# Kernel optimization log

Measured on AMD Instinct MI355X. Metric: run time of the kernel, lower is better.

## Reference

```python
import jax, jax.numpy as jnp
import numpy as np

TEMPERATURE = 0.5
EPS = 1e-8  # matches torch CosineSimilarity eps


def setup_inputs() -> dict:
    key = jax.random.key(0)
    k1, k2 = jax.random.split(key)
    N, D = 4096, 256
    z1 = jax.random.normal(k1, (N, D), dtype=jnp.float32)
    z2 = jax.random.normal(k2, (N, D), dtype=jnp.float32)
    return {"z1": z1, "z2": z2}


def reference(z1, z2):
    N = z1.shape[0]
    z = jnp.concatenate([z1, z2], axis=0)            # [2N, D]
    norm = jnp.linalg.norm(z, axis=-1, keepdims=True)
    zn = z / jnp.maximum(norm, EPS)                  # L2-normalized
    sim = (zn @ zn.T) / TEMPERATURE                  # [2N, 2N] cosine sim / temp
    # mask self-similarity on the diagonal
    diag = jnp.eye(2 * N, dtype=bool)
    sim = jnp.where(diag, -jnp.inf, sim)
    # positive pair labels: row i pairs with i+N (first half) or i-N (second half)
    labels = jnp.concatenate([jnp.arange(N) + N, jnp.arange(N)])
    logp = jax.nn.log_softmax(sim, axis=-1)
    loss = -jnp.mean(logp[jnp.arange(2 * N), labels])
    return loss
```

## Files before the change

### kernel.cpp

```cpp
#include <hip/hip_runtime.h>
#include <hip/hip_bf16.h>


#define NROWS 8192
#define NHALF 4096
#define DDIM  256

typedef __bf16 bf16;
typedef __bf16 bf16x4 __attribute__((ext_vector_type(4)));
typedef __bf16 bf16x8 __attribute__((ext_vector_type(8)));
typedef float  f32x4  __attribute__((ext_vector_type(4)));

__constant__ const float kTwoLog2e = 2.8853900817779268f;
__constant__ const float kLn2      = 0.6931471805599453f;

__device__ __forceinline__ const float* zrow(const float* z1, const float* z2, int r) {
  return (r < NHALF) ? (z1 + (size_t)r * DDIM) : (z2 + (size_t)(r - NHALF) * DDIM);
}

__global__ void k_normalize(const float* __restrict__ z1, const float* __restrict__ z2,
                            bf16* __restrict__ zn, float* __restrict__ invn,
                            float* __restrict__ rowsum) {
  const int wave = threadIdx.x >> 6, lane = threadIdx.x & 63;
  const int row = blockIdx.x * 4 + wave;
  const float* src = zrow(z1, z2, row);
  f32x4 v = *(const f32x4*)(src + lane * 4);
  float ss = v.x * v.x + v.y * v.y + v.z * v.z + v.w * v.w;
#pragma unroll
  for (int off = 1; off < 64; off <<= 1) ss += __shfl_xor(ss, off);
  const float inv = 1.0f / fmaxf(sqrtf(ss), 1e-8f);
  bf16x4 o;
  o.x = (bf16)(v.x * inv); o.y = (bf16)(v.y * inv);
  o.z = (bf16)(v.z * inv); o.w = (bf16)(v.w * inv);
  *(bf16x4*)(zn + (size_t)row * DDIM + lane * 4) = o;
  if (lane == 0) { invn[row] = inv; rowsum[row] = 0.0f; }
}

#define BMG 128
#define NTILES 2080

typedef const __attribute__((address_space(1))) unsigned int* as1_u32p;
typedef __attribute__((address_space(3))) unsigned int* as3_u32p;

__device__ __forceinline__ void load_lds16(const void* g, void* l) {
  __builtin_amdgcn_global_load_lds((as1_u32p)g, (as3_u32p)l, 16, 0, 0);
}

__global__ __launch_bounds__(256, 2) void k_gram(const bf16* __restrict__ zn,
                                                 float* __restrict__ rowsum) {
  __shared__ __align__(16) unsigned char ldsb[2][64 * 512];
  const int tid  = threadIdx.x;
  const int wave = tid >> 6, lane = tid & 63;
  const int quad = lane >> 4, l15 = lane & 15;

  const int kb = blockIdx.x;
  int I = (int)((129.0f - sqrtf((float)(16641 - 8 * kb))) * 0.5f);
  while ((I + 1) * (129 - (I + 1)) / 2 <= kb) ++I;
  while (I * (129 - I) / 2 > kb) --I;
  const int J = I + (kb - I * (129 - I) / 2);
  const bool diag = (I == J);
  const int R0 = I * BMG + wave * 32;
  const int C0 = J * BMG;

  {
    const unsigned char* s0 = (const unsigned char*)(zn + (size_t)C0 * DDIM);
#pragma unroll
    for (int j = 0; j < 8; ++j) {
      const int p = (wave * 8 + j) * 64 + lane;
      const int r = p >> 5;
      const int q = (p & 31) ^ (r & 15);
      load_lds16(s0 + r * 512 + q * 16, &ldsb[0][(wave * 8 + j) * 1024]);
    }
  }

  bf16x8 a[2][8];
#pragma unroll
  for (int s = 0; s < 2; ++s) {
    const bf16x8* ap = (const bf16x8*)(zn + (size_t)(R0 + s * 16 + l15) * DDIM);
#pragma unroll
    for (int kk = 0; kk < 8; ++kk) a[s][kk] = ap[kk * 4 + quad];
  }

  {
    const unsigned char* s1 = (const unsigned char*)(zn + (size_t)(C0 + 64) * DDIM);
#pragma unroll
    for (int j = 0; j < 8; ++j) {
      const int p = (wave * 8 + j) * 64 + lane;
      const int r = p >> 5;
      const int q = (p & 31) ^ (r & 15);
      load_lds16(s1 + r * 512 + q * 16, &ldsb[1][(wave * 8 + j) * 1024]);
    }
  }
  __builtin_amdgcn_sched_barrier(0);

  float sum[2][4] = {{0.f, 0.f, 0.f, 0.f}, {0.f, 0.f, 0.f, 0.f}};
  float csum[2][4];
  const f32x4 zero4 = {0.f, 0.f, 0.f, 0.f};

#pragma unroll
  for (int h = 0; h < 2; ++h) {
    if (h == 0) {
      asm volatile("s_waitcnt vmcnt(8)" ::: "memory");
    } else {
      asm volatile("s_waitcnt vmcnt(0)" ::: "memory");
    }
    __builtin_amdgcn_s_barrier();
    __builtin_amdgcn_sched_barrier(0);

    const unsigned char* bp = ldsb[h];

    f32x4 acc[2][4];
#pragma unroll
    for (int s = 0; s < 2; ++s)
#pragma unroll
      for (int cs = 0; cs < 4; ++cs) acc[s][cs] = zero4;

    __builtin_amdgcn_s_setprio(1);
#pragma unroll
    for (int kk = 0; kk < 8; ++kk) {
      bf16x8 b[4];
#pragma unroll
      for (int cs = 0; cs < 4; ++cs) {
        const int rb = cs * 16 + l15;
        const int sl = (kk * 4 + quad) ^ (rb & 15);
        b[cs] = *(const bf16x8*)(bp + rb * 512 + sl * 16);
      }
#pragma unroll
      for (int s = 0; s < 2; ++s)
#pragma unroll
        for (int cs = 0; cs < 4; ++cs)
          acc[s][cs] =
              __builtin_amdgcn_mfma_f32_16x16x32_bf16(a[s][kk], b[cs], acc[s][cs], 0, 0, 0);
    }
    __builtin_amdgcn_s_setprio(0);

#pragma unroll
    for (int cs = 0; cs < 4; ++cs) {
      float c = 0.f;
#pragma unroll
      for (int s = 0; s < 2; ++s)
#pragma unroll
        for (int r = 0; r < 4; ++r) {
          const float e = __builtin_amdgcn_exp2f(acc[s][cs][r] * kTwoLog2e);
          sum[s][r] += e;
          c += e;
        }
      csum[h][cs] = c;
    }
  }

#pragma unroll
  for (int s = 0; s < 2; ++s)
#pragma unroll
    for (int r = 0; r < 4; ++r) {
      float v = sum[s][r];
      v += __shfl_xor(v, 1); v += __shfl_xor(v, 2);
      v += __shfl_xor(v, 4); v += __shfl_xor(v, 8);
      if (l15 == 0) atomicAdd(&rowsum[R0 + s * 16 + quad * 4 + r], v);
    }

  if (!diag) {
#pragma unroll
    for (int h = 0; h < 2; ++h)
#pragma unroll
      for (int cs = 0; cs < 4; ++cs) {
        float v = csum[h][cs];
        v += __shfl_xor(v, 16); v += __shfl_xor(v, 32);
        if (quad == 0) atomicAdd(&rowsum[C0 + h * 64 + cs * 16 + l15], v);
      }
  }
}

__global__ void k_finalize(const float* __restrict__ z1, const float* __restrict__ z2,
                           const bf16* __restrict__ zn, const float* __restrict__ invn,
                           const float* __restrict__ rowsum, float* __restrict__ contrib) {
  const int wave = threadIdx.x >> 6, lane = threadIdx.x & 63;
  const int row = blockIdx.x * 4 + wave;
  const int pr = (row < NHALF) ? row + NHALF : row - NHALF;

  f32x4 a4 = *(const f32x4*)(zrow(z1, z2, row) + lane * 4);
  f32x4 b4 = *(const f32x4*)(zrow(z1, z2, pr) + lane * 4);
  bf16x4 nb = *(const bf16x4*)(zn + (size_t)row * DDIM + lane * 4);

  float pd = a4.x * b4.x + a4.y * b4.y + a4.z * b4.z + a4.w * b4.w;
  float f0 = (float)nb.x, f1 = (float)nb.y, f2 = (float)nb.z, f3 = (float)nb.w;
  float nd = f0 * f0 + f1 * f1 + f2 * f2 + f3 * f3;
#pragma unroll
  for (int off = 1; off < 64; off <<= 1) {
    pd += __shfl_xor(pd, off);
    nd += __shfl_xor(nd, off);
  }
  if (lane == 0) {
    const float p = 2.0f * pd * invn[row] * invn[pr];
    const float dexp = __builtin_amdgcn_exp2f(kTwoLog2e * nd);
    const float lse = __builtin_amdgcn_logf(rowsum[row] - dexp) * kLn2;
    contrib[row] = lse - p;
  }
}

__global__ void k_reduce(const float* __restrict__ contrib, float* __restrict__ out) {
  const int wave = threadIdx.x >> 6, lane = threadIdx.x & 63;
  float acc = 0.0f;
  for (int i = threadIdx.x; i < NROWS; i += 256) acc += contrib[i];
#pragma unroll
  for (int off = 1; off < 64; off <<= 1) acc += __shfl_xor(acc, off);
  __shared__ float wsum[4];
  if (lane == 0) wsum[wave] = acc;
  __syncthreads();
  if (threadIdx.x == 0)
    out[0] = (wsum[0] + wsum[1] + wsum[2] + wsum[3]) * (1.0f / (float)NROWS);
}

extern "C" void kernel_launch(void* const* d_in, const int* in_sizes, int n_in,
                              void* d_out, int out_size, void* d_ws, size_t ws_size,
                              hipStream_t stream) {
  const float* z1 = (const float*)d_in[0];
  const float* z2 = (const float*)d_in[1];
  unsigned char* ws = (unsigned char*)d_ws;

  bf16* zn = (bf16*)ws;
  float* invn = (float*)(ws + (size_t)NROWS * DDIM * sizeof(bf16));
  float* rowsum = invn + NROWS;
  float* contrib = rowsum + NROWS;

  hipLaunchKernelGGL(k_normalize, dim3(NROWS / 4), dim3(256), 0, stream, z1, z2, zn, invn, rowsum);
  hipLaunchKernelGGL(k_gram, dim3(NTILES), dim3(256), 0, stream, zn, rowsum);
  hipLaunchKernelGGL(k_finalize, dim3(NROWS / 4), dim3(256), 0, stream, z1, z2, zn, invn, rowsum,
                     contrib);
  hipLaunchKernelGGL(k_reduce, dim3(1), dim3(256), 0, stream, contrib, (float*)d_out);
}
```

Measured before the change: 118.9 us.

## Make gram blocks persistent over a cyclic tile band with double-buffered LDS pipeline

The symmetric gram kernel moves from 2080 one-tile blocks to 512 blocks. Each block keeps its A row-block in registers and walks a cyclic band of column tiles, streaming B tiles through double-buffered LDS with asynchronous loads. This amortises A loads and launch overhead and overlaps DMA with MFMA, but adds per-tile barriers and column atomics. Separately, the final reduction kernel is removed: finalize now reduces per block and atomically adds into the output, which normalize zeroes.

```diff
diff --git a/kernel.cpp b/kernel.cpp
--- a/kernel.cpp
+++ b/kernel.cpp
@@ -20,7 +20,7 @@
 
 __global__ void k_normalize(const float* __restrict__ z1, const float* __restrict__ z2,
                             bf16* __restrict__ zn, float* __restrict__ invn,
-                            float* __restrict__ rowsum) {
+                            float* __restrict__ rowsum, float* __restrict__ out) {
   const int wave = threadIdx.x >> 6, lane = threadIdx.x & 63;
   const int row = blockIdx.x * 4 + wave;
   const float* src = zrow(z1, z2, row);
@@ -34,16 +34,17 @@
   o.z = (bf16)(v.z * inv); o.w = (bf16)(v.w * inv);
   *(bf16x4*)(zn + (size_t)row * DDIM + lane * 4) = o;
   if (lane == 0) { invn[row] = inv; rowsum[row] = 0.0f; }
-}
-
-#define BMG 128
-#define NTILES 2080
+  if (blockIdx.x == 0 && threadIdx.x == 0) out[0] = 0.0f;
+}
+
+#define NBLK 512
 
 typedef const __attribute__((address_space(1))) unsigned int* as1_u32p;
 typedef __attribute__((address_space(3))) unsigned int* as3_u32p;
 
 __device__ __forceinline__ void load_lds16(const void* g, void* l) {
-  __builtin_amdgcn_global_load_lds((as1_u32p)g, (as3_u32p)l, 16, 0, 0);
+  __builtin_amdgcn_global_lo\
+ad_lds((as1_u32p)g, (as3_u32p)l, 16, 0, 0);
 }
 
 __global__ __launch_bounds__(256, 2) void k_gram(const bf16* __restrict__ zn,
@@ -53,25 +54,30 @@
   const int wave = tid >> 6, lane = tid & 63;
   const int quad = lane >> 4, l15 = lane & 15;
 
-  const int kb = blockIdx.x;
-  int I = (int)((129.0f - sqrtf((float)(16641 - 8 * kb))) * 0.5f);
-  while ((I + 1) * (129 - (I + 1)) / 2 <= kb) ++I;
-  while (I * (129 - I) / 2 > kb) --I;
-  const int J = I + (kb - I * (129 - I) / 2);
-  const bool diag = (I == J);
-  const int R0 = I * BMG + wave * 32;
-  const int C0 = J * BMG;
-
-  {
-    const unsigned char* s0 = (const unsigned char*)(zn + (size_t)C0 * DDIM);
+  const int I      = blockIdx.x >> 3;
+  const int chunk  = blockIdx.x & 7;
+  const int base_d = chunk * 4;
+  const int n      = (chunk == 7 && I < 32) ? 10 : 8;
+  const int R0     = I * 128 + wave * 32;
+
+  auto cbase = [&](int t) -> int {
+    const int d = base_d + (t >> 1);
+    const int J = (I + d) & 63;
+    return J * 128 + (t & 1) * 64;
+  };
+  auto issue_dma = [&](int t, int b) {
+    const unsigned char* s = (const unsigned char*)(zn + (size_t)cbase(t) * DDIM);
 #pragma unroll
     for (int j = 0; j < 8; ++j) {
       const int p = (wave * 8 + j) * 64 + lane;
       const int r = p >> 5;
       const int q = (p & 31) ^ (r & 15);
-      load_lds16(s0 + r * 512 + q * 16, &ldsb[0][(wave * 8 + j) * 1024]);
-    }
-  }
+      load_lds16(s + r * 512 + q * 16, &ldsb[b][(wave * 8 + j) * 1024]);
+    }
+  };
+
+  issue_dma(0, 0);
+  __builtin_amdgcn_sched_barrier(0);
 
   bf16x8 a[2][8];
 #pragma unroll
@@ -80,34 +86,21 @@
 #pragma unroll
     for (int kk = 0; kk < 8; ++kk) a[s][kk] = ap[kk * 4 + quad];
   }
-
-  {
-    const unsigned char* s1 = (const unsigned char*)(zn + (size_t)(C0 + 64) * DDIM);
-#pragma unroll
-    for (int j = 0; j < 8; ++j) {
-      const int p = (wave * 8 + j) * 64 + lane;
-      const int r = p >> 5;
-      const int q = (p & 31) ^ (r & 15);
-      load_lds16(s1 + r * 512 + q * 16, &ldsb[1][(wave * 8 + j) * 1024]);
-    }
-  }
   __builtin_amdgcn_sched_barrier(0);
 
+  issue_dma(1, 1);
+  __builtin_amdgcn_sched_barrier(0);
+
   float sum[2][4] = {{0.f, 0.f, 0.f, 0.f}, {0.f, 0.f, 0.f, 0.f}};
-  float csum[2][4];
   const f32x4 zero4 = {0.f, 0.f, 0.f, 0.f};
 
-#pragma unroll
-  for (int h = 0; h < 2; ++h) {
-    if (h == 0) {
-      asm volatile("s_waitcnt vmcnt(8)" ::: "memory");
-    } else {
-      asm volatile("s_waitcnt vmcnt(0)" ::: "memory");
-    }
+  for (int t = 0; t < n; ++t) {
+    if (t == n - 1) asm volatile("s_waitcnt vmcnt(0)" ::: "memory");
+    else            asm volatile("s_waitcnt vmcnt(8)" ::: "memory");
     __builtin_amdgcn_s_barrier();
     __builtin_amdgcn_sched_barrier(0);
 
-    const unsigned char* bp = ldsb[h];
+    const unsigned char* bp = ldsb[t & 1];
 
     f32x4 acc[2][4];
 #pragma unroll
@@ -134,6 +127,8 @@
     }
     __builtin_amdgcn_s_setprio(0);
 
+    const bool dg = (chunk == 0 && t < 2);
+    const int cb = cbase(t);
 #pragma unroll
     for (int cs = 0; cs < 4; ++cs) {
       float c = 0.f;
@@ -145,7 +140,17 @@
           sum[s][r] += e;
           c += e;
         }
-      csum[h][cs] = c;
+      if (!dg) {
+        c += __shfl_xor(c, 16); c += __shfl_xor(c, 32);
+        if (quad == 0) atomicAdd(&rowsum[cb + cs * 16 + l15], c);
+      }
+    }
+
+    __builtin_amdgcn_s_barrier();
+    __builtin_amdgcn_sched_barrier(0);
+    if (t + 2 < n) {
+      issue_dma(t + 2, t & 1);
+      __builtin_amdgcn_sched_barrier(0);
     }
   }
 
@@ -158,22 +163,11 @@
       v += __shfl_xor(v, 4); v += __shfl_xor(v, 8);
       if (l15 == 0) atomicAdd(&rowsum[R0 + s * 16 + quad * 4 + r], v);
     }
-
-  if (!diag) {
-#pragma unroll
-    for (int h = 0; h < 2; ++h)
-#pragma unroll
-      for (int cs = 0; cs < 4; ++cs) {
-        float v = csum[h][cs];
-        v += __shfl_xor(v, 16); v += __shfl_xor(v, 32);
-        if (quad == 0) atomicAdd(&rowsum[C0 + h * 64 + cs * 16 + l15], v);
-      }
-  }
 }
 
 __global__ void k_finalize(const float* __restrict__ z1, const float* __restrict__ z2,
                            const bf16* __restrict__ zn, const float* __restrict__ invn,
-                           const float* __restrict__ rowsum, float* __restrict__ contrib) {
+                           const float* __restrict__ rowsum, float* __restrict__ out) {
   const int wave = threadIdx.x >> 6, lane = threadIdx.x & 63;
   const int row = blockIdx.x * 4 + wave;
   const int pr = (row < NHALF) ? row + NHALF : row - NHALF;
@@ -190,25 +184,16 @@
     pd += __shfl_xor(pd, off);
     nd += __shfl_xor(nd, off);
   }
+  __shared__ float wsum[4];
   if (lane == 0) {
     const float p = 2.0f * pd * invn[row] * invn[pr];
     const float dexp = __builtin_amdgcn_exp2f(kTwoLog2e * nd);
     const float lse = __builtin_amdgcn_logf(rowsum[row] - dexp) * kLn2;
-    contrib[row] = lse - p;
-  }
-}
-
-__global__ void k_reduce(const float* __restrict__ contrib, float* __restrict__ out) {
-  const int wave = threadIdx.x >> 6, lane = threadIdx.x & 63;
-  float acc = 0.0f;
-  for (int i = threadIdx.x; i < NROWS; i += 256) acc += contrib[i];
-#pragma unroll
-  for (int off = 1; off < 64; off <<= 1) acc += __shfl_xor(acc, off);
-  __shared__ float wsum[4];
-  if (lane == 0) wsum[wave] = acc;
+    wsum[wave] = lse - p;
+  }
   __syncthreads();
   if (threadIdx.x == 0)
-    out[0] = (wsum[0] + wsum[1] + wsum[2] + wsum[3]) * (1.0f / (float)NROWS);
+    atomicAdd(out, (wsum[0] + wsum[1] + wsum[2] + wsum[3]) * (1.0f / (float)NROWS));
 }
 
 extern "C" void kernel_launch(void* const* d_in, const int* in_sizes, int n_in,
@@ -221,11 +206,11 @@
   bf16* zn = (bf16*)ws;
   float* invn = (float*)(ws + (size_t)NROWS * DDIM * sizeof(bf16));
   float* rowsum = invn + NROWS;
-  float* contrib = rowsum + NROWS;
-
-  hipLaunchKernelGGL(k_normalize, dim3(NROWS / 4), dim3(256), 0, stream, z1, z2, zn, invn, rowsum);
-  hipLaunchKernelGGL(k_gram, dim3(NTILES), dim3(256), 0, stream, zn, rowsum);
+  float* out = (float*)d_out;
+
+  hipLaunchKernelGGL(k_normalize, dim3(NROWS / 4), dim3(256), 0, stream, z1, z2, zn, invn, rowsum,
+                     out);
+  hipLaunchKernelGGL(k_gram, dim3(NBLK), dim3(256), 0, stream, zn, rowsum);
   hipLaunchKernelGGL(k_finalize, dim3(NROWS / 4), dim3(256), 0, stream, z1, z2, zn, invn, rowsum,
-                     contrib);
-  hipLaunchKernelGGL(k_reduce, dim3(1), dim3(256), 0, stream, contrib, (float*)d_out);
-}
+                     out);
+}
```

New measurement: 117.0 us. About the same (-1.5%).
